# Optimization experiments

Measured on AMD Instinct MI355X. Metric: run time of the kernel, lower is better.

Reference implementation:

```python
import jax, jax.numpy as jnp
import numpy as np

N = 50000      # nodes
D = 64         # hidden size
E = 800000     # edges (avg degree 16)
DEPTH = 2      # GraphSAGE layers


def setup_inputs() -> dict:
    key = jax.random.key(0)
    k1, k2, k3, k4 = jax.random.split(key, 4)
    x = jax.random.normal(k1, (N, D), dtype=jnp.float32)
    edge_src = jax.random.randint(k2, (E,), 0, N)
    edge_dst = jax.random.randint(k3, (E,), 0, N)
    # per-layer weight applied to concat([h_self, h_neigh]) -> (D, 2D)
    W = jax.random.normal(k4, (DEPTH, D, 2 * D), dtype=jnp.float32) * (1.0 / np.sqrt(2 * D))
    return {"x": x, "W": W, "edge_src": edge_src, "edge_dst": edge_dst}


def reference(x, W, edge_src, edge_dst):
    n = x.shape[0]
    # neighbor counts for mean aggregation (isolated nodes -> 0 aggregate)
    deg = jax.ops.segment_sum(jnp.ones_like(edge_dst, dtype=x.dtype), edge_dst, num_segments=n)
    inv_deg = jnp.where(deg > 0, 1.0 / jnp.maximum(deg, 1.0), 0.0)  # [N]
    h = x
    for k in range(W.shape[0]):
        # mean of neighbor features: gather on src, scatter-add on dst
        neigh = jax.ops.segment_sum(h[edge_src], edge_dst, num_segments=n) * inv_deg[:, None]
        z = jnp.concatenate([h, neigh], axis=-1)          # [N, 2D]
        new = jax.nn.relu(jnp.einsum('nd,hd->nh', z, W[k]))  # W_k @ concat per node
        norm = jnp.linalg.norm(new, axis=-1, keepdims=True)
        h = new / jnp.maximum(norm, 1e-12)                 # L2 normalize per node
    return h
```

## Files before the change

### kernel.cpp

```cpp
#include <hip/hip_runtime.h>

#define HD 64

typedef short  bf16x8 __attribute__((ext_vector_type(8)));
typedef float  f32x4  __attribute__((ext_vector_type(4)));

__device__ inline float bf2f(ushort u) {
    unsigned x = ((unsigned)u) << 16;
    return __builtin_bit_cast(float, x);
}
__device__ inline ushort f2bf(float f) {
    unsigned u = __builtin_bit_cast(unsigned, f);
    u += 0x7fffu + ((u >> 16) & 1u);
    return (ushort)(u >> 16);
}

__global__ void prep_kernel(const float4* __restrict__ x, ushort4* __restrict__ hb, int xn4,
                            const float4* __restrict__ W, ushort4* __restrict__ Wb, int wn4,
                            int4* __restrict__ deg4, int dn4) {
    int i = blockIdx.x * blockDim.x + threadIdx.x;
    if (i < xn4) {
        float4 v = x[i];
        ushort4 o; o.x = f2bf(v.x); o.y = f2bf(v.y); o.z = f2bf(v.z); o.w = f2bf(v.w);
        hb[i] = o;
        return;
    }
    int j = i - xn4;
    if (j < wn4) {
        float4 v = W[j];
        ushort4 o; o.x = f2bf(v.x); o.y = f2bf(v.y); o.z = f2bf(v.z); o.w = f2bf(v.w);
        Wb[j] = o;
        return;
    }
    int k = j - wn4;
    if (k < dn4) deg4[k] = int4{0, 0, 0, 0};
}

__global__ void deg_part_kernel(const int* __restrict__ dst, int* __restrict__ deg,
                                int E, int N) {
    const int g = blockIdx.x & 7;
    const int per = (N + 7) / 8;
    const int lo = g * per;
    const int hi = min(N, lo + per);
    const int nb = gridDim.x >> 3;
    const int b = blockIdx.x >> 3;
    for (int e = b * blockDim.x + threadIdx.x; e < E; e += nb * blockDim.x) {
        int d = dst[e];
        if (d >= lo && d < hi) atomicAdd(&deg[d], 1);
    }
}

__global__ __launch_bounds__(1024) void scanA_kernel(const int* __restrict__ deg,
                                                     int* __restrict__ excl,
                                                     int* __restrict__ bsum, int N) {
    const int tid = threadIdx.x, lane = tid & 63, wid = tid >> 6;
    const int i = blockIdx.x * 1024 + tid;
    int v = (i < N) ? deg[i] : 0;
    int s = v;
#pragma unroll
    for (int off = 1; off < 64; off <<= 1) {
        int t = __shfl_up(s, off, 64);
        if (lane >= off) s += t;
    }
    __shared__ int wtot[16], woff[16];
    if (lane == 63) wtot[wid] = s;
    __syncthreads();
    if (wid == 0 && lane < 16) {
        int t = wtot[lane];
        int ss = t;
#pragma unroll
        for (int off = 1; off < 16; off <<= 1) {
            int u = __shfl_up(ss, off, 64);
            if (lane >= off) ss += u;
        }
        woff[lane] = ss - t;
        if (lane == 15) bsum[blockIdx.x] = ss;
    }
    __syncthreads();
    if (i < N) excl[i] = woff[wid] + (s - v);
}

__global__ __launch_bounds__(1024) void scanC_kernel(const int* __restrict__ excl,
                                                     const int* __restrict__ bsum,
                                                     const int* __restrict__ deg,
                                                     int* __restrict__ row_start,
                                                     int* __restrict__ cursor,
                                                     float* __restrict__ inv_deg,
                                                     int N, int E, int NB) {
    __shared__ int boff_s;
    const int tid = threadIdx.x;
    if (tid < 64) {
        int lane = tid;
        int v = (lane < NB) ? bsum[lane] : 0;
        int s = v;
#pragma unroll
        for (int off = 1; off < 64; off <<= 1) {
            int t = __shfl_up(s, off, 64);
            if (lane >= off) s += t;
        }
        if (lane == (int)blockIdx.x) boff_s = s - v;
    }
    __syncthreads();
    const int boff = boff_s;
    int i = blockIdx.x * 1024 + tid;
    if (i < N) {
        int e = excl[i] + boff;
        row_start[i] = e;
        cursor[i] = e;
        int d = deg[i];
        inv_deg[i] = (d > 0) ? 1.0f / (float)d : 0.0f;
    }
    if (blockIdx.x == 0 && tid == 0) row_start[N] = E;
}

__global__ void fill_part_kernel(const int* __restrict__ src, const int* __restrict__ dst,
                                 int* __restrict__ cursor, int* __restrict__ csr,
                                 int E, int N) {
    const int g = blockIdx.x & 7;
    const int per = (N + 7) / 8;
    const int lo = g * per;
    const int hi = min(N, lo + per);
    const int nb = gridDim.x >> 3;
    const int b = blockIdx.x >> 3;
    for (int e = b * blockDim.x + threadIdx.x; e < E; e += nb * blockDim.x) {
        int d = dst[e];
        if (d >= lo && d < hi) {
            int p = atomicAdd(&cursor[d], 1);
            csr[p] = src[e];
        }
    }
}

__global__ __launch_bounds__(256, 8) void agg_kernel(
    const ushort* __restrict__ hb, const int* __restrict__ row_start,
    const int* __restrict__ csr, const float* __restrict__ inv_deg,
    ushort* __restrict__ neighb, int N) {
    const int wv = (blockIdx.x * blockDim.x + threadIdx.x) >> 6;
    const int lane = threadIdx.x & 63;
    if (wv >= N) return;
    const int rs = row_start[wv];
    const int re = row_start[wv + 1];
    const int grp = lane >> 4;
    const int sub = (lane & 15) << 2;

    float a0 = 0.f, a1 = 0.f, a2 = 0.f, a3 = 0.f;
    float b0 = 0.f, b1 = 0.f, b2 = 0.f, b3 = 0.f;
    int j = rs;
    while (j < re) {
        int take = re - j;
        if (take > 64) take = 64;
        int idx = (lane < take) ? csr[j + lane] : 0;
        int i = 0;
        for (; i + 8 <= take; i += 8) {
            int s0 = __shfl(idx, i + grp, 64);
            int s1 = __shfl(idx, i + 4 + grp, 64);
            ushort4 v0 = *(const ushort4*)&hb[(long long)s0 * HD + sub];
            ushort4 v1 = *(const ushort4*)&hb[(long long)s1 * HD + sub];
            a0 += bf2f(v0.x); a1 += bf2f(v0.y); a2 += bf2f(v0.z); a3 += bf2f(v0.w);
            b0 += bf2f(v1.x); b1 += bf2f(v1.y); b2 += bf2f(v1.z); b3 += bf2f(v1.w);
        }
        for (; i < take; i += 4) {
            int p = i + grp;
            int s = __shfl(idx, p < take ? p : 0, 64);
            if (p < take) {
                ushort4 v = *(const ushort4*)&hb[(long long)s * HD + sub];
                a0 += bf2f(v.x); a1 += bf2f(v.y); a2 += bf2f(v.z); a3 += bf2f(v.w);
            }
        }
        j += take;
    }
    a0 += b0; a1 += b1; a2 += b2; a3 += b3;
    a0 += __shfl_xor(a0, 16, 64); a0 += __shfl_xor(a0, 32, 64);
    a1 += __shfl_xor(a1, 16, 64); a1 += __shfl_xor(a1, 32, 64);
    a2 += __shfl_xor(a2, 16, 64); a2 += __shfl_xor(a2, 32, 64);
    a3 += __shfl_xor(a3, 16, 64); a3 += __shfl_xor(a3, 32, 64);
    if (grp == 0) {
        float inv = inv_deg[wv];
        ushort4 o;
        o.x = f2bf(a0 * inv); o.y = f2bf(a1 * inv);
        o.z = f2bf(a2 * inv); o.w = f2bf(a3 * inv);
        *(ushort4*)&neighb[(long long)wv * HD + sub] = o;
    }
}

__global__ __launch_bounds__(256) void gemm_mfma_kernel(
    const ushort* __restrict__ hb, const ushort* __restrict__ nbf,
    const ushort* __restrict__ Wb, float* __restrict__ out,
    ushort* __restrict__ hb_out, int N, int last) {
    const int lane = threadIdx.x & 63;
    const int w = threadIdx.x >> 6;
    const int base = blockIdx.x * 64 + w * 16;
    const int m = lane & 15;
    const int kq = lane >> 4;
    int anode = base + m;
    if (anode > N - 1) anode = N - 1;
    const long long arow = (long long)anode * HD;

    f32x4 acc[4] = {{0.f,0.f,0.f,0.f},{0.f,0.f,0.f,0.f},{0.f,0.f,0.f,0.f},{0.f,0.f,0.f,0.f}};
#pragma unroll
    for (int kk = 0; kk < 4; ++kk) {
        const ushort* ap = (kk < 2 ? hb : nbf) + arow + (kk & 1) * 32 + kq * 8;
        bf16x8 a = *(const bf16x8*)ap;
        const ushort* bp = Wb + (long long)m * 128 + kk * 32 + kq * 8;
#pragma unroll
        for (int t = 0; t < 4; ++t) {
            bf16x8 b = *(const bf16x8*)(bp + (long long)t * 16 * 128);
            acc[t] = __builtin_amdgcn_mfma_f32_16x16x32_bf16(a, b, acc[t], 0, 0, 0);
        }
    }

    float sq[4] = {0.f, 0.f, 0.f, 0.f};
#pragma unroll
    for (int t = 0; t < 4; ++t)
#pragma unroll
        for (int r = 0; r < 4; ++r) {
            float v = fmaxf(acc[t][r], 0.f);
            acc[t][r] = v;
            sq[r] += v * v;
        }
#pragma unroll
    for (int off = 1; off < 16; off <<= 1)
#pragma unroll
        for (int r = 0; r < 4; ++r) sq[r] += __shfl_xor(sq[r], off, 64);

    float scl[4];
#pragma unroll
    for (int r = 0; r < 4; ++r) scl[r] = 1.f / fmaxf(sqrtf(sq[r]), 1e-12f);

    if (last) {
#pragma unroll
        for (int r = 0; r < 4; ++r) {
            int node = base + kq * 4 + r;
            if (node < N) {
#pragma unroll
                for (int t = 0; t < 4; ++t)
                    out[(long long)node * HD + t * 16 + m] = acc[t][r] * scl[r];
            }
        }
    } else {
#pragma unroll
        for (int r = 0; r < 4; ++r) {
            int node = base + kq * 4 + r;
            if (node < N) {
#pragma unroll
                for (int t = 0; t < 4; ++t)
                    hb_out[(long long)node * HD + t * 16 + m] = f2bf(acc[t][r] * scl[r]);
            }
        }
    }
}

extern "C" void kernel_launch(void* const* d_in, const int* in_sizes, int n_in,
                              void* d_out, int out_size, void* d_ws, size_t ws_size,
                              hipStream_t stream) {
    const float* x    = (const float*)d_in[0];
    const float* W    = (const float*)d_in[1];
    const int*   esrc = (const int*)d_in[2];
    const int*   edst = (const int*)d_in[3];
    float* out = (float*)d_out;

    const int N = in_sizes[0] / HD;
    const int E = in_sizes[2];
    const int DEPTH = in_sizes[1] / (HD * 2 * HD);
    const int NB = (N + 1023) / 1024;

    auto align256 = [](size_t v) { return (v + 255) & ~(size_t)255; };
    char* ws = (char*)d_ws;
    int*    deg       = (int*)ws;     ws += align256((size_t)(N + 8) * 4);
    int*    excl      = (int*)ws;     ws += align256((size_t)N * 4);
    int*    bsum      = (int*)ws;     ws += align256(64 * 4);
    int*    row_start = (int*)ws;     ws += align256((size_t)(N + 1) * 4);
    int*    cursor    = (int*)ws;     ws += align256((size_t)N * 4);
    float*  inv_deg   = (float*)ws;   ws += align256((size_t)N * 4);
    int*    csr       = (int*)ws;     ws += align256((size_t)E * 4);
    ushort* hb0       = (ushort*)ws;  ws += align256((size_t)N * HD * 2);
    ushort* hb1       = (ushort*)ws;  ws += align256((size_t)N * HD * 2);
    ushort* neighb    = (ushort*)ws;  ws += align256((size_t)N * HD * 2);
    ushort* Wb        = (ushort*)ws;

    int xn4 = N * HD / 4;
    int wn4 = DEPTH * HD * 2 * HD / 4;
    int dn4 = (N + 3) / 4;
    int ptot = xn4 + wn4 + dn4;
    prep_kernel<<<(ptot + 255) / 256, 256, 0, stream>>>(
        (const float4*)x, (ushort4*)hb0, xn4,
        (const float4*)W, (ushort4*)Wb, wn4,
        (int4*)deg, dn4);

    deg_part_kernel<<<2048, 256, 0, stream>>>(edst, deg, E, N);
    scanA_kernel<<<NB, 1024, 0, stream>>>(deg, excl, bsum, N);
    scanC_kernel<<<NB, 1024, 0, stream>>>(excl, bsum, deg, row_start, cursor, inv_deg, N, E, NB);
    fill_part_kernel<<<2048, 256, 0, stream>>>(esrc, edst, cursor, csr, E, N);

    ushort* hb_cur = hb0;
    ushort* hb_nxt = hb1;
    for (int k = 0; k < DEPTH; ++k) {
        int last = (k == DEPTH - 1) ? 1 : 0;
        agg_kernel<<<(N * 64 + 255) / 256, 256, 0, stream>>>(hb_cur, row_start, csr,
                                                             inv_deg, neighb, N);
        gemm_mfma_kernel<<<(N + 63) / 64, 256, 0, stream>>>(hb_cur, neighb,
                                                            Wb + (size_t)k * HD * 2 * HD,
                                                            out, hb_nxt, N, last);
        ushort* t = hb_cur; hb_cur = hb_nxt; hb_nxt = t;
    }
}
```

Before: 157.7 us.

## Fuse neighbor aggregation into MFMA layer kernel, dropping neighb buffer

Merges the per-layer aggregation and GEMM kernels into a single kernel. Each lane gathers its node's neighbors directly into registers laid out as MFMA A-operand fragments, then the kernel runs the matmul, ReLU and normalisation. This removes the neighb round trip through global memory and one launch per layer. The cost is that each 16-node wave loops to the maximum degree in the wave with masked loads, which adds wasted work on skewed degrees. Each lane also now gathers 32 contiguous bytes per neighbor, where before 16 lanes shared one coalesced row load.

```diff
diff --git a/kernel.cpp b/kernel.cpp
--- a/kernel.cpp
+++ b/kernel.cpp
@@ -131,80 +131,74 @@
     }
 }
 
-__global__ __launch_bounds__(256, 8) void agg_kernel(
+__global__ __launch_bounds__(256) void layer_mfma_kernel(
     const ushort* __restrict__ hb, const int* __restrict__ row_start,
     const int* __restrict__ csr, const float* __restrict__ inv_deg,
-    ushort* __restrict__ neighb, int N) {
-    const int wv = (blockIdx.x * blockDim.x + threadIdx.x) >> 6;
-    const int lane = threadIdx.x & 63;
-    if (wv >= N) return;
-    const int rs = row_start[wv];
-    const int re = row_start[wv + 1];
-    const int grp = lane >> 4;
-    const int sub = (lane & 15) << 2;
-
-    float a0 = 0.f, a1 = 0.f, a2 = 0.f, a3 = 0.f;
-    float b0 = 0.f, b1 = 0.f, b2 = 0.f, b3 = 0.f;
-    int j = rs;
-    while (j < re) {
-        int take = re - j;
-        if (take > 64) take = 64;
-        int idx = (lane < take) ? csr[j + lane] : 0;
-        int i = 0;
-        for (; i + 8 <= take; i += 8) {
-            int s0 = __shfl(idx, i + grp, 64);
-            int s1 = __shfl(idx, i + 4 + grp, 64);
-            ushort4 v0 = *(const ushort4*)&hb[(long long)s0 * HD + sub];
-            ushort4 v1 = *(const ushort4*)&hb[(long long)s1 * HD + sub];
-            a0 += bf2f(v0.x); a1 += bf2f(v0.y); a2 += bf2f(v0.z); a3 += bf2f(v0.w);
-            b0 += bf2f(v1.x); b1 += bf2f(v1.y); b2 += bf2f(v1.z); b3 += bf2f(v1.w);
-        }
-        for (; i < take; i += 4) {
-            int p = i + grp;
-            int s = __shfl(idx, p < take ? p : 0, 64);
-            if (p < take) {
-                ushort4 v = *(const ushort4*)&hb[(long long)s * HD + sub];
-                a0 += bf2f(v.x); a1 += bf2f(v.y); a2 += bf2f(v.z); a3 += bf2f(v.w);
-            }
-        }
-        j += take;
-    }
-    a0 += b0; a1 += b1; a2 += b2; a3 += b3;
-    a0 += __shfl_xor(a0, 16, 64); a0 += __shfl_xor(a0, 32, 64);
-    a1 += __shfl_xor(a1, 16, 64); a1 += __shfl_xor(a1, 32, 64);
-    a2 += __shfl_xor(a2, 16, 64); a2 += __shfl_xor(a2, 32, 64);
-    a3 += __shfl_xor(a3, 16, 64); a3 += __shfl_xor(a3, 32, 64);
-    if (grp == 0) {
-        float inv = inv_deg[wv];
-        ushort4 o;
-        o.x = f2bf(a0 * inv); o.y = f2bf(a1 * inv);
-        o.z = f2bf(a2 * inv); o.w = f2bf(a3 * inv);
-        *(ushort4*)&neighb[(long long)wv * HD + sub] = o;
-    }
-}
-
-__global__ __launch_bounds__(256) void gemm_mfma_kernel(
-    const ushort* __restrict__ hb, const ushort* __restrict__ nbf,
     const ushort* __restrict__ Wb, float* __restrict__ out,
-    ushort* __restrict__ hb_out, int N, int last) {
+    ushort* __restrict__ hb_out, int N, int E, int last) {
     const int lane = threadIdx.x & 63;
     const int w = threadIdx.x >> 6;
     const int base = blockIdx.x * 64 + w * 16;
     const int m = lane & 15;
     const int kq = lane >> 4;
-    int anode = base + m;
-    if (anode > N - 1) anode = N - 1;
-    const long long arow = (long long)anode * HD;
+    int cnode = base + m;
+    if (cnode > N - 1) cnode = N - 1;
+    const int arow = cnode << 6;
+
+    bf16x8 a0 = *(const bf16x8*)(hb + arow + kq * 8);
+    bf16x8 a1 = *(const bf16x8*)(hb + arow + 32 + kq * 8);
+
+    const int r0 = row_start[cnode];
+    const int dg = row_start[cnode + 1] - r0;
+    const float inv = inv_deg[cnode];
+
+    int dgmax = dg;
+#pragma unroll
+    for (int off = 1; off < 64; off <<= 1)
+        dgmax = max(dgmax, __shfl_xor(dgmax, off, 64));
+
+    float accL[8] = {0.f,0.f,0.f,0.f,0.f,0.f,0.f,0.f};
+    float accH[8] = {0.f,0.f,0.f,0.f,0.f,0.f,0.f,0.f};
+    const int Em1 = E - 1;
+    for (int j = 0; j < dgmax; j += 2) {
+        int p0 = r0 + j;       if (p0 > Em1) p0 = Em1;
+        int p1 = r0 + j + 1;   if (p1 > Em1) p1 = Em1;
+        int s0 = csr[p0];
+        int s1 = csr[p1];
+        float w0 = (j < dg) ? 1.f : 0.f;
+        float w1 = (j + 1 < dg) ? 1.f : 0.f;
+        const ushort* q0 = hb + (s0 << 6) + kq * 8;
+        const ushort* q1 = hb + (s1 << 6) + kq * 8;
+        bf16x8 l0 = *(const bf16x8*)q0;
+        bf16x8 h0 = *(const bf16x8*)(q0 + 32);
+        bf16x8 l1 = *(const bf16x8*)q1;
+        bf16x8 h1 = *(const bf16x8*)(q1 + 32);
+#pragma unroll
+        for (int i = 0; i < 8; ++i) {
+            accL[i] = fmaf(w0, bf2f((ushort)l0[i]), accL[i]);
+            accH[i] = fmaf(w0, bf2f((ushort)h0[i]), accH[i]);
+        }
+#pragma unroll
+        for (int i = 0; i < 8; ++i) {
+            accL[i] = fmaf(w1, bf2f((ushort)l1[i]), accL[i]);
+            accH[i] = fmaf(w1, bf2f((ushort)h1[i]), accH[i]);
+        }
+    }
+    bf16x8 a2, a3;
+#pragma unroll
+    for (int i = 0; i < 8; ++i) {
+        a2[i] = (short)f2bf(accL[i] * inv);
+        a3[i] = (short)f2bf(accH[i] * inv);
+    }
 
     f32x4 acc[4] = {{0.f,0.f,0.f,0.f},{0.f,0.f,0.f,0.f},{0.f,0.f,0.f,0.f},{0.f,0.f,0.f,0.f}};
 #pragma unroll
     for (int kk = 0; kk < 4; ++kk) {
-        const ushort* ap = (kk < 2 ? hb : nbf) + arow + (kk & 1) * 32 + kq * 8;
-        bf16x8 a = *(const bf16x8*)ap;
-        const ushort* bp = Wb + (long long)m * 128 + kk * 32 + kq * 8;
+        bf16x8 a = (kk == 0) ? a0 : (kk == 1) ? a1 : (kk == 2) ? a2 : a3;
+        const ushort* bp = Wb + m * 128 + kk * 32 + kq * 8;
 #pragma unroll
         for (int t = 0; t < 4; ++t) {
-            bf16x8 b = *(const bf16x8*)(bp + (long long)t * 16 * 128);
+            bf16x8 b = *(const bf16x8*)(bp + t * 16 * 128);
             acc[t] = __builtin_amdgcn_mfma_f32_16x16x32_bf16(a, b, acc[t], 0, 0, 0);
         }
     }
@@ -275,7 +269,6 @@
     int*    csr       = (int*)ws;     ws += align256((size_t)E * 4);
     ushort* hb0       = (ushort*)ws;  ws += align256((size_t)N * HD * 2);
     ushort* hb1       = (ushort*)ws;  ws += align256((size_t)N * HD * 2);
-    ushort* neighb    = (ushort*)ws;  ws += align256((size_t)N * HD * 2);
     ushort* Wb        = (ushort*)ws;
 
     int xn4 = N * HD / 4;
@@ -296,11 +289,9 @@
     ushort* hb_nxt = hb1;
     for (int k = 0; k < DEPTH; ++k) {
         int last = (k == DEPTH - 1) ? 1 : 0;
-        agg_kernel<<<(N * 64 + 255) / 256, 256, 0, stream>>>(hb_cur, row_start, csr,
-                                                             inv_deg, neighb, N);
-        gemm_mfma_kernel<<<(N + 63) / 64, 256, 0, stream>>>(hb_cur, neighb,
-                                                            Wb + (size_t)k * HD * 2 * HD,
-                                                            out, hb_nxt, N, last);
+        layer_mfma_kernel<<<(N + 63) / 64, 256, 0, stream>>>(
+            hb_cur, row_start, csr, inv_deg,
+            Wb + (size_t)k * HD * 2 * HD, out, hb_nxt, N, E, last);
         ushort* t = hb_cur; hb_cur = hb_nxt; hb_nxt = t;
     }
 }
```

Result: slower. 167.3 us (+6.0%).

## Fuse neighbor aggregation and MFMA GEMM into one per-layer kernel via LDS

Applied to the files above, without the earlier changes.

Merges the aggregation and GEMM kernels into a single layer kernel. Each wave aggregates 16 nodes serially and writes the bf16 means into a swizzled shared-memory tile, which the MFMA stage then reads directly. This removes the global round trip of the neighbor buffer and one launch per layer. In exchange, each wave now walks 16 nodes one after another, so there are far fewer waves in flight to hide gather latency.

```diff
diff --git a/kernel.cpp b/kernel.cpp
--- a/kernel.cpp
+++ b/kernel.cpp
@@ -131,80 +131,89 @@
     }
 }
 
-__global__ __launch_bounds__(256, 8) void agg_kernel(
+__global__ __launch_bounds__(256) void layer_kernel(
     const ushort* __restrict__ hb, const int* __restrict__ row_start,
     const int* __restrict__ csr, const float* __restrict__ inv_deg,
-    ushort* __restrict__ neighb, int N) {
-    const int wv = (blockIdx.x * blockDim.x + threadIdx.x) >> 6;
-    const int lane = threadIdx.x & 63;
-    if (wv >= N) return;
-    const int rs = row_start[wv];
-    const int re = row_start[wv + 1];
+    const ushort* __restrict__ Wb, float* __restrict__ out,
+    ushort* __restrict__ hb_out, int N, int last) {
+    __shared__ ushort nl[64 * 64];
+    const int tid = threadIdx.x;
+    const int lane = tid & 63;
+    const int w = tid >> 6;
+    const int base = blockIdx.x * 64;
+
     const int grp = lane >> 4;
     const int sub = (lane & 15) << 2;
-
-    float a0 = 0.f, a1 = 0.f, a2 = 0.f, a3 = 0.f;
-    float b0 = 0.f, b1 = 0.f, b2 = 0.f, b3 = 0.f;
-    int j = rs;
-    while (j < re) {
-        int take = re - j;
-        if (take > 64) take = 64;
-        int idx = (lane < take) ? csr[j + lane] : 0;
-        int i = 0;
-        for (; i + 8 <= take; i += 8) {
-            int s0 = __shfl(idx, i + grp, 64);
-            int s1 = __shfl(idx, i + 4 + grp, 64);
-            ushort4 v0 = *(const ushort4*)&hb[(long long)s0 * HD + sub];
-            ushort4 v1 = *(const ushort4*)&hb[(long long)s1 * HD + sub];
-            a0 += bf2f(v0.x); a1 += bf2f(v0.y); a2 += bf2f(v0.z); a3 += bf2f(v0.w);
-            b0 += bf2f(v1.x); b1 += bf2f(v1.y); b2 += bf2f(v1.z); b3 += bf2f(v1.w);
-        }
-        for (; i < take; i += 4) {
-            int p = i + grp;
-            int s = __shfl(idx, p < take ? p : 0, 64);
-            if (p < take) {
-                ushort4 v = *(const ushort4*)&hb[(long long)s * HD + sub];
-                a0 += bf2f(v.x); a1 += bf2f(v.y); a2 += bf2f(v.z); a3 += bf2f(v.w);
+    for (int n = 0; n < 16; ++n) {
+        int node = base + w * 16 + n;
+        if (node >= N) break;
+        const int rs = row_start[node];
+        const int re = row_start[node + 1];
+        float a0 = 0.f, a1 = 0.f, a2 = 0.f, a3 = 0.f;
+        float b0 = 0.f, b1 = 0.f, b2 = 0.f, b3 = 0.f;
+        int j = rs;
+        while (j < re) {
+            int take = re - j;
+            if (take > 64) take = 64;
+            int idx = (lane < take) ? csr[j + lane] : 0;
+            int i = 0;
+            for (; i + 8 <= take; i += 8) {
+                int s0 = __shfl(idx, i + grp, 64);
+                int s1 = __shfl(idx, i + 4 + grp, 64);
+                ushort4 v0 = *(const ushort4*)&hb[(s0 << 6) + sub];
+                ushort4 v1 = *(const ushort4*)&hb[(s1 << 6) + sub];
+                a0 += bf2f(v0.x); a1 += bf2f(v0.y); a2 += bf2f(v0.z); a3 += bf2f(v0.w);
+                b0 += bf2f(v1.x); b1 += bf2f(v1.y); b2 += bf2f(v1.z); b3 += bf2f(v1.w);
             }
-        }
-        j += take;
-    }
-    a0 += b0; a1 += b1; a2 += b2; a3 += b3;
-    a0 += __shfl_xor(a0, 16, 64); a0 += __shfl_xor(a0, 32, 64);
-    a1 += __shfl_xor(a1, 16, 64); a1 += __shfl_xor(a1, 32, 64);
-    a2 += __shfl_xor(a2, 16, 64); a2 += __shfl_xor(a2, 32, 64);
-    a3 += __shfl_xor(a3, 16, 64); a3 += __shfl_xor(a3, 32, 64);
-    if (grp == 0) {
-        float inv = inv_deg[wv];
-        ushort4 o;
-        o.x = f2bf(a0 * inv); o.y = f2bf(a1 * inv);
-        o.z = f2bf(a2 * inv); o.w = f2bf(a3 * inv);
-        *(ushort4*)&neighb[(long long)wv * HD + sub] = o;
-    }
-}
-
-__global__ __launch_bounds__(256) void gemm_mfma_kernel(
-    const ushort* __restrict__ hb, const ushort* __restrict__ nbf,
-    const ushort* __restrict__ Wb, float* __restrict__ out,
-    ushort* __restrict__ hb_out, int N, int last) {
-    const int lane = threadIdx.x & 63;
-    const int w = threadIdx.x >> 6;
-    const int base = blockIdx.x * 64 + w * 16;
+            for (; i < take; i += 4) {
+                int p = i + grp;
+                int s = __shfl(idx, p < take ? p : 0, 64);
+                if (p < take) {
+                    ushort4 v = *(const ushort4*)&hb[(s << 6) + sub];
+                    a0 += bf2f(v.x); a1 += bf2f(v.y); a2 += bf2f(v.z); a3 += bf2f(v.w);
+                }
+            }
+            j += take;
+        }
+        a0 += b0; a1 += b1; a2 += b2; a3 += b3;
+        a0 += __shfl_xor(a0, 16, 64); a0 += __shfl_xor(a0, 32, 64);
+        a1 += __shfl_xor(a1, 16, 64); a1 += __shfl_xor(a1, 32, 64);
+        a2 += __shfl_xor(a2, 16, 64); a2 += __shfl_xor(a2, 32, 64);
+        a3 += __shfl_xor(a3, 16, 64); a3 += __shfl_xor(a3, 32, 64);
+        if (grp == 0) {
+            float inv = inv_deg[node];
+            int ln = node - base;
+            int gi = sub >> 3;
+            int half = sub & 7;
+            ushort4 o;
+            o.x = f2bf(a0 * inv); o.y = f2bf(a1 * inv);
+            o.z = f2bf(a2 * inv); o.w = f2bf(a3 * inv);
+            *(ushort4*)&nl[ln * 64 + ((gi ^ (ln & 7)) << 3) + half] = o;
+        }
+    }
+    __syncthreads();
+
     const int m = lane & 15;
     const int kq = lane >> 4;
-    int anode = base + m;
-    if (anode > N - 1) anode = N - 1;
-    const long long arow = (long long)anode * HD;
+    const int wbase = base + w * 16;
+    int cnode = wbase + m;
+    if (cnode > N - 1) cnode = N - 1;
+    const int arow = cnode << 6;
+    const int ln = w * 16 + m;
+
+    bf16x8 af0 = *(const bf16x8*)(hb + arow + kq * 8);
+    bf16x8 af1 = *(const bf16x8*)(hb + arow + 32 + kq * 8);
+    bf16x8 af2 = *(const bf16x8*)&nl[ln * 64 + ((kq ^ (ln & 7)) << 3)];
+    bf16x8 af3 = *(const bf16x8*)&nl[ln * 64 + (((4 + kq) ^ (ln & 7)) << 3)];
 
     f32x4 acc[4] = {{0.f,0.f,0.f,0.f},{0.f,0.f,0.f,0.f},{0.f,0.f,0.f,0.f},{0.f,0.f,0.f,0.f}};
 #pragma unroll
     for (int kk = 0; kk < 4; ++kk) {
-        const ushort* ap = (kk < 2 ? hb : nbf) + arow + (kk & 1) * 32 + kq * 8;
-        bf16x8 a = *(const bf16x8*)ap;
-        const ushort* bp = Wb + (long long)m * 128 + kk * 32 + kq * 8;
+        bf16x8 a = (kk == 0) ? af0 : (kk == 1) ? af1 : (kk == 2) ? af2 : af3;
+        const ushort* bp = Wb + m * 128 + kk * 32 + kq * 8;
 #pragma unroll
         for (int t = 0; t < 4; ++t) {
-            bf16x8 b = *(const bf16x8*)(bp + (long long)t * 16 * 128);
+            bf16x8 b = *(const bf16x8*)(bp + t * 16 * 128);
             acc[t] = __builtin_amdgcn_mfma_f32_16x16x32_bf16(a, b, acc[t], 0, 0, 0);
         }
     }
@@ -230,7 +239,7 @@
     if (last) {
 #pragma unroll
         for (int r = 0; r < 4; ++r) {
-            int node = base + kq * 4 + r;
+            int node = wbase + kq * 4 + r;
             if (node < N) {
 #pragma unroll
                 for (int t = 0; t < 4; ++t)
@@ -240,7 +249,7 @@
     } else {
 #pragma unroll
         for (int r = 0; r < 4; ++r) {
-            int node = base + kq * 4 + r;
+            int node = wbase + kq * 4 + r;
             if (node < N) {
 #pragma unroll
                 for (int t = 0; t < 4; ++t)
@@ -275,7 +284,6 @@
     int*    csr       = (int*)ws;     ws += align256((size_t)E * 4);
     ushort* hb0       = (ushort*)ws;  ws += align256((size_t)N * HD * 2);
     ushort* hb1       = (ushort*)ws;  ws += align256((size_t)N * HD * 2);
-    ushort* neighb    = (ushort*)ws;  ws += align256((size_t)N * HD * 2);
     ushort* Wb        = (ushort*)ws;
 
     int xn4 = N * HD / 4;
@@ -296,11 +304,9 @@
     ushort* hb_nxt = hb1;
     for (int k = 0; k < DEPTH; ++k) {
         int last = (k == DEPTH - 1) ? 1 : 0;
-        agg_kernel<<<(N * 64 + 255) / 256, 256, 0, stream>>>(hb_cur, row_start, csr,
-                                                             inv_deg, neighb, N);
-        gemm_mfma_kernel<<<(N + 63) / 64, 256, 0, stream>>>(hb_cur, neighb,
-                                                            Wb + (size_t)k * HD * 2 * HD,
-                                                            out, hb_nxt, N, last);
+        layer_kernel<<<(N + 63) / 64, 256, 0, stream>>>(
+            hb_cur, row_start, csr, inv_deg,
+            Wb + (size_t)k * HD * 2 * HD, out, hb_nxt, N, last);
         ushort* t = hb_cur; hb_cur = hb_nxt; hb_nxt = t;
     }
 }
```

New measurement: 186.0 us. 17.9% more time.

## Fuse CSR build into one persistent kernel with grid barriers; unroll aggregation

Applied to the files above, without the earlier changes.

Replaces the four CSR-construction kernels (degree count, two scan passes, fill) with a single 64-block persistent kernel that separates phases with atomic-counter grid barriers, removing three launch gaps and the excl buffer. The aggregation loop gains a 16-neighbor unrolled path with four independent accumulator sets to raise memory-level parallelism, and index math switches to 32-bit shifts. The tradeoff is far fewer threads (64×1024) for the edge-scanning atomic phases than the previous 2048×256 grids. The barrier also assumes all 64 blocks are co-resident.

```diff
diff --git a/kernel.cpp b/kernel.cpp
--- a/kernel.cpp
+++ b/kernel.cpp
@@ -1,6 +1,7 @@
 #include <hip/hip_runtime.h>
 
 #define HD 64
+#define NBLD 64
 
 typedef short  bf16x8 __attribute__((ext_vector_type(8)));
 typedef float  f32x4  __attribute__((ext_vector_type(4)));
@@ -17,7 +18,7 @@
 
 __global__ void prep_kernel(const float4* __restrict__ x, ushort4* __restrict__ hb, int xn4,
                             const float4* __restrict__ W, ushort4* __restrict__ Wb, int wn4,
-                            int4* __restrict__ deg4, int dn4) {
+                            int4* __restrict__ deg4, int dn4, int4* __restrict__ bar4) {
     int i = blockIdx.x * blockDim.x + threadIdx.x;
     if (i < xn4) {
         float4 v = x[i];
@@ -33,100 +34,108 @@
         return;
     }
     int k = j - wn4;
-    if (k < dn4) deg4[k] = int4{0, 0, 0, 0};
-}
-
-__global__ void deg_part_kernel(const int* __restrict__ dst, int* __restrict__ deg,
-                                int E, int N) {
-    const int g = blockIdx.x & 7;
+    if (k < dn4) { deg4[k] = int4{0, 0, 0, 0}; return; }
+    int m = k - dn4;
+    if (m < 4) bar4[m] = int4{0, 0, 0, 0};
+}
+
+__device__ inline void gridbar(int* bar, int slot) {
+    __syncthreads();
+    if (threadIdx.x == 0) {
+        __threadfence();
+        atomicAdd(&bar[slot], 1);
+        while (__hip_atomic_load(&bar[slot], __ATOMIC_ACQUIRE,
+                                 __HIP_MEMORY_SCOPE_AGENT) < NBLD) {}
+    }
+    __syncthreads();
+}
+
+__global__ __launch_bounds__(1024, 4) void build_kernel(
+    const int* __restrict__ esrc, const int* __restrict__ edst,
+    int* __restrict__ deg, int* __restrict__ bsum,
+    int* __restrict__ row_start, int* __restrict__ cursor,
+    float* __restrict__ inv_deg, int* __restrict__ csr,
+    int* __restrict__ bar, int N, int E, int NBsc) {
+    const int tid = threadIdx.x, lane = tid & 63, wid = tid >> 6;
     const int per = (N + 7) / 8;
-    const int lo = g * per;
-    const int hi = min(N, lo + per);
-    const int nb = gridDim.x >> 3;
-    const int b = blockIdx.x >> 3;
-    for (int e = b * blockDim.x + threadIdx.x; e < E; e += nb * blockDim.x) {
-        int d = dst[e];
-        if (d >= lo && d < hi) atomicAdd(&deg[d], 1);
-    }
-}
-
-__global__ __launch_bounds__(1024) void scanA_kernel(const int* __restrict__ deg,
-                                                     int* __restrict__ excl,
-                                                     int* __restrict__ bsum, int N) {
-    const int tid = threadIdx.x, lane = tid & 63, wid = tid >> 6;
-    const int i = blockIdx.x * 1024 + tid;
-    int v = (i < N) ? deg[i] : 0;
-    int s = v;
-#pragma unroll
-    for (int off = 1; off < 64; off <<= 1) {
-        int t = __shfl_up(s, off, 64);
-        if (lane >= off) s += t;
-    }
+
+    {
+        const int g = blockIdx.x & 7;
+        const int lo = g * per;
+        const int hi = min(N, lo + per);
+        const int b = blockIdx.x >> 3;
+        for (int e = b * 1024 + tid; e < E; e += 8 * 1024) {
+            int d = edst[e];
+            if (d >= lo && d < hi) atomicAdd(&deg[d], 1);
+        }
+    }
+    gridbar(bar, 0);
+
     __shared__ int wtot[16], woff[16];
-    if (lane == 63) wtot[wid] = s;
-    __syncthreads();
-    if (wid == 0 && lane < 16) {
-        int t = wtot[lane];
-        int ss = t;
-#pragma unroll
-        for (int off = 1; off < 16; off <<= 1) {
-            int u = __shfl_up(ss, off, 64);
-            if (lane >= off) ss += u;
-        }
-        woff[lane] = ss - t;
-        if (lane == 15) bsum[blockIdx.x] = ss;
-    }
-    __syncthreads();
-    if (i < N) excl[i] = woff[wid] + (s - v);
-}
-
-__global__ __launch_bounds__(1024) void scanC_kernel(const int* __restrict__ excl,
-                                                     const int* __restrict__ bsum,
-                                                     const int* __restrict__ deg,
-                                                     int* __restrict__ row_start,
-                                                     int* __restrict__ cursor,
-                                                     float* __restrict__ inv_deg,
-                                                     int N, int E, int NB) {
-    __shared__ int boff_s;
-    const int tid = threadIdx.x;
-    if (tid < 64) {
-        int lane = tid;
-        int v = (lane < NB) ? bsum[lane] : 0;
+    if ((int)blockIdx.x < NBsc) {
+        int i = blockIdx.x * 1024 + tid;
+        int v = (i < N) ? deg[i] : 0;
         int s = v;
 #pragma unroll
         for (int off = 1; off < 64; off <<= 1) {
             int t = __shfl_up(s, off, 64);
             if (lane >= off) s += t;
         }
-        if (lane == (int)blockIdx.x) boff_s = s - v;
-    }
-    __syncthreads();
-    const int boff = boff_s;
-    int i = blockIdx.x * 1024 + tid;
-    if (i < N) {
-        int e = excl[i] + boff;
-        row_start[i] = e;
-        cursor[i] = e;
-        int d = deg[i];
-        inv_deg[i] = (d > 0) ? 1.0f / (float)d : 0.0f;
-    }
-    if (blockIdx.x == 0 && tid == 0) row_start[N] = E;
-}
-
-__global__ void fill_part_kernel(const int* __restrict__ src, const int* __restrict__ dst,
-                                 int* __restrict__ cursor, int* __restrict__ csr,
-                                 int E, int N) {
-    const int g = blockIdx.x & 7;
-    const int per = (N + 7) / 8;
-    const int lo = g * per;
-    const int hi = min(N, lo + per);
-    const int nb = gridDim.x >> 3;
-    const int b = blockIdx.x >> 3;
-    for (int e = b * blockDim.x + threadIdx.x; e < E; e += nb * blockDim.x) {
-        int d = dst[e];
-        if (d >= lo && d < hi) {
-            int p = atomicAdd(&cursor[d], 1);
-            csr[p] = src[e];
+        if (lane == 63) wtot[wid] = s;
+        __syncthreads();
+        if (wid == 0 && lane < 16) {
+            int t = wtot[lane];
+            int ss = t;
+#pragma unroll
+            for (int off = 1; off < 16; off <<= 1) {
+                int u = __shfl_up(ss, off, 64);
+                if (lane >= off) ss += u;
+            }
+            woff[lane] = ss - t;
+            if (lane == 15) bsum[blockIdx.x] = ss;
+        }
+        __syncthreads();
+        if (i < N) row_start[i] = woff[wid] + (s - v);
+    }
+    gridbar(bar, 1);
+
+    if ((int)blockIdx.x < NBsc) {
+        __shared__ int boff_s;
+        if (tid < 64) {
+            int v = (lane < NBsc) ? bsum[lane] : 0;
+            int s = v;
+#pragma unroll
+            for (int off = 1; off < 64; off <<= 1) {
+                int t = __shfl_up(s, off, 64);
+                if (lane >= off) s += t;
+            }
+            if (lane == (int)blockIdx.x) boff_s = s - v;
+        }
+        __syncthreads();
+        const int boff = boff_s;
+        int i = blockIdx.x * 1024 + tid;
+        if (i < N) {
+            int e = row_start[i] + boff;
+            row_start[i] = e;
+            cursor[i] = e;
+            int d = deg[i];
+            inv_deg[i] = (d > 0) ? 1.0f / (float)d : 0.0f;
+        }
+        if (blockIdx.x == 0 && tid == 0) row_start[N] = E;
+    }
+    gridbar(bar, 2);
+
+    {
+        const int g = blockIdx.x & 7;
+        const int lo = g * per;
+        const int hi = min(N, lo + per);
+        const int b = blockIdx.x >> 3;
+        for (int e = b * 1024 + tid; e < E; e += 8 * 1024) {
+            int d = edst[e];
+            if (d >= lo && d < hi) {
+                int p = atomicAdd(&cursor[d], 1);
+                csr[p] = esrc[e];
+            }
         }
     }
 }
@@ -145,17 +154,33 @@
 
     float a0 = 0.f, a1 = 0.f, a2 = 0.f, a3 = 0.f;
     float b0 = 0.f, b1 = 0.f, b2 = 0.f, b3 = 0.f;
+    float c0 = 0.f, c1 = 0.f, c2 = 0.f, c3 = 0.f;
+    float d0 = 0.f, d1 = 0.f, d2 = 0.f, d3 = 0.f;
     int j = rs;
     while (j < re) {
         int take = re - j;
         if (take > 64) take = 64;
         int idx = (lane < take) ? csr[j + lane] : 0;
         int i = 0;
+        for (; i + 16 <= take; i += 16) {
+            int s0 = __shfl(idx, i + grp, 64);
+            int s1 = __shfl(idx, i + 4 + grp, 64);
+            int s2 = __shfl(idx, i + 8 + grp, 64);
+            int s3 = __shfl(idx, i + 12 + grp, 64);
+            ushort4 v0 = *(const ushort4*)&hb[(s0 << 6) + sub];
+            ushort4 v1 = *(const ushort4*)&hb[(s1 << 6) + sub];
+            ushort4 v2 = *(const ushort4*)&hb[(s2 << 6) + sub];
+            ushort4 v3 = *(const ushort4*)&hb[(s3 << 6) + sub];
+            a0 += bf2f(v0.x); a1 += bf2f(v0.y); a2 += bf2f(v0.z); a3 += bf2f(v0.w);
+            b0 += bf2f(v1.x); b1 += bf2f(v1.y); b2 += bf2f(v1.z); b3 += bf2f(v1.w);
+            c0 += bf2f(v2.x); c1 += bf2f(v2.y); c2 += bf2f(v2.z); c3 += bf2f(v2.w);
+            d0 += bf2f(v3.x); d1 += bf2f(v3.y); d2 += bf2f(v3.z); d3 += bf2f(v3.w);
+        }
         for (; i + 8 <= take; i += 8) {
             int s0 = __shfl(idx, i + grp, 64);
             int s1 = __shfl(idx, i + 4 + grp, 64);
-            ushort4 v0 = *(const ushort4*)&hb[(long long)s0 * HD + sub];
-            ushort4 v1 = *(const ushort4*)&hb[(long long)s1 * HD + sub];
+            ushort4 v0 = *(const ushort4*)&hb[(s0 << 6) + sub];
+            ushort4 v1 = *(const ushort4*)&hb[(s1 << 6) + sub];
             a0 += bf2f(v0.x); a1 += bf2f(v0.y); a2 += bf2f(v0.z); a3 += bf2f(v0.w);
             b0 += bf2f(v1.x); b1 += bf2f(v1.y); b2 += bf2f(v1.z); b3 += bf2f(v1.w);
         }
@@ -163,13 +188,14 @@
             int p = i + grp;
             int s = __shfl(idx, p < take ? p : 0, 64);
             if (p < take) {
-                ushort4 v = *(const ushort4*)&hb[(long long)s * HD + sub];
+                ushort4 v = *(const ushort4*)&hb[(s << 6) + sub];
                 a0 += bf2f(v.x); a1 += bf2f(v.y); a2 += bf2f(v.z); a3 += bf2f(v.w);
             }
         }
         j += take;
     }
-    a0 += b0; a1 += b1; a2 += b2; a3 += b3;
+    a0 += b0 + c0 + d0; a1 += b1 + c1 + d1;
+    a2 += b2 + c2 + d2; a3 += b3 + c3 + d3;
     a0 += __shfl_xor(a0, 16, 64); a0 += __shfl_xor(a0, 32, 64);
     a1 += __shfl_xor(a1, 16, 64); a1 += __shfl_xor(a1, 32, 64);
     a2 += __shfl_xor(a2, 16, 64); a2 += __shfl_xor(a2, 32, 64);
@@ -179,7 +205,7 @@
         ushort4 o;
         o.x = f2bf(a0 * inv); o.y = f2bf(a1 * inv);
         o.z = f2bf(a2 * inv); o.w = f2bf(a3 * inv);
-        *(ushort4*)&neighb[(long long)wv * HD + sub] = o;
+        *(ushort4*)&neighb[(wv << 6) + sub] = o;
     }
 }
 
@@ -262,12 +288,12 @@
     const int N = in_sizes[0] / HD;
     const int E = in_sizes[2];
     const int DEPTH = in_sizes[1] / (HD * 2 * HD);
-    const int NB = (N + 1023) / 1024;
+    const int NBsc = (N + 1023) / 1024;
 
     auto align256 = [](size_t v) { return (v + 255) & ~(size_t)255; };
     char* ws = (char*)d_ws;
     int*    deg       = (int*)ws;     ws += align256((size_t)(N + 8) * 4);
-    int*    excl      = (int*)ws;     ws += align256((size_t)N * 4);
+    int*    bar       = (int*)ws;     ws += align256(16 * 4);
     int*    bsum      = (int*)ws;     ws += align256(64 * 4);
     int*    row_start = (int*)ws;     ws += align256((size_t)(N + 1) * 4);
     int*    cursor    = (int*)ws;     ws += align256((size_t)N * 4);
@@ -280,17 +306,15 @@
 
     int xn4 = N * HD / 4;
     int wn4 = DEPTH * HD * 2 * HD / 4;
-    int dn4 = (N + 3) / 4;
-    int ptot = xn4 + wn4 + dn4;
+    int dn4 = (N + 8) / 4;
+    int ptot = xn4 + wn4 + dn4 + 4;
     prep_kernel<<<(ptot + 255) / 256, 256, 0, stream>>>(
         (const float4*)x, (ushort4*)hb0, xn4,
         (const float4*)W, (ushort4*)Wb, wn4,
-        (int4*)deg, dn4);
-
-    deg_part_kernel<<<2048, 256, 0, stream>>>(edst, deg, E, N);
-    scanA_kernel<<<NB, 1024, 0, stream>>>(deg, excl, bsum, N);
-    scanC_kernel<<<NB, 1024, 0, stream>>>(excl, bsum, deg, row_start, cursor, inv_deg, N, E, NB);
-    fill_part_kernel<<<2048, 256, 0, stream>>>(esrc, edst, cursor, csr, E, N);
+        (int4*)deg, dn4, (int4*)bar);
+
+    build_kernel<<<NBLD, 1024, 0, stream>>>(esrc, edst, deg, bsum, row_start,
+                                            cursor, inv_deg, csr, bar, N, E, NBsc);
 
     ushort* hb_cur = hb0;
     ushort* hb_nxt = hb1;
```

Result: slower. 234.5 us (+48.7%).
